# Performance work log

Hardware: AMD Instinct MI355X
Metric: run time of the kernel (lower is better)

## Reference

```python
import jax, jax.numpy as jnp
import numpy as np

D = 128
NQ = 25  # r2d2 quantized AP: 25 triangular bins over similarity range [0, 1]


def grid_sample_bilinear(img, grid):
    """F.grid_sample, mode='bilinear', padding_mode='zeros', align_corners=False.
    img: (B,C,H,W), grid: (B,Hg,Wg,2) in [-1,1] (x, y order). -> (B,C,Hg,Wg)"""
    B, C, H, W = img.shape
    gx = ((grid[..., 0] + 1.0) * W - 1.0) * 0.5  # (B,Hg,Wg) unnormalized x
    gy = ((grid[..., 1] + 1.0) * H - 1.0) * 0.5
    x0f = jnp.floor(gx)
    y0f = jnp.floor(gy)
    wx1 = gx - x0f
    wy1 = gy - y0f
    x0 = x0f.astype(jnp.int32)
    y0 = y0f.astype(jnp.int32)

    def gather(yi, xi):
        valid = ((xi >= 0) & (xi < W) & (yi >= 0) & (yi < H)).astype(img.dtype)
        xc = jnp.clip(xi, 0, W - 1)
        yc = jnp.clip(yi, 0, H - 1)
        v = jax.vmap(lambda im, y, x: im[:, y, x])(img, yc, xc)  # (B,C,Hg,Wg)
        return v * valid[:, None]

    out = (gather(y0, x0) * ((1 - wy1) * (1 - wx1))[:, None]
           + gather(y0, x0 + 1) * ((1 - wy1) * wx1)[:, None]
           + gather(y0 + 1, x0) * (wy1 * (1 - wx1))[:, None]
           + gather(y0 + 1, x0 + 1) * (wy1 * wx1)[:, None])
    return out


def quantized_ap(sim, lab):
    """r2d2 QAPLoss: soft-histogram differentiable AP.
    sim: (B,N,M) similarities, lab: (B,N,M) binary labels (float). -> (B,N) AP per query."""
    a = jnp.float32(NQ - 1)                 # slope; bin width = 1/a over gap [0,1]
    c = jnp.linspace(1.0, 0.0, NQ, dtype=sim.dtype)  # bin centers, descending score
    # triangular kernel membership: relu(1 - a*|s - c|), shape (B,N,Q,M)
    q = jnp.maximum(0.0, 1.0 - a * jnp.abs(sim[:, :, None, :] - c[None, None, :, None]))
    nbs = q.sum(-1)                          # (B,N,Q) soft count per bin
    rec = (q * lab[:, :, None, :]).sum(-1)   # (B,N,Q) soft positive count per bin
    prec = jnp.cumsum(rec, -1) / (1e-16 + jnp.cumsum(nbs, -1))
    rec = rec / rec.sum(-1, keepdims=True)
    return (prec * rec).sum(-1)              # (B,N)


def setup_inputs() -> dict:
    key = jax.random.key(0)
    k1, k2, k3, k4, k5 = jax.random.split(key, 5)
    B, H, W = 2, 32, 32
    d1 = jax.random.normal(k1, (B, D, H, W), dtype=jnp.float32)
    d2 = jax.random.normal(k2, (B, D, H, W), dtype=jnp.float32)
    # L2-normalize over channels (r2d2 descriptors are unit-norm -> sims in [-1,1])
    d1 = d1 / jnp.linalg.norm(d1, axis=1, keepdims=True)
    d2 = d2 / jnp.linalg.norm(d2, axis=1, keepdims=True)
    rel = jax.random.uniform(k3, (B, 1, H, W), dtype=jnp.float32)
    grid = jax.random.uniform(k4, (B, H, W, 2), dtype=jnp.float32) * 1.8 - 0.9  # in [-0.9,0.9]
    label = jax.random.randint(k5, (B, H, W, H, W), 0, 2, dtype=jnp.int32)
    return {"desc1": d1, "desc2": d2, "reliability": rel, "grid": grid, "label": label}


def reference(desc1, desc2, reliability, grid, label):
    B, C, H, W = desc1.shape
    d2w = grid_sample_bilinear(desc2, grid)           # warp image2 descriptors
    q = desc1.reshape(B, C, H * W).transpose(0, 2, 1)  # (B,N,C)
    db = d2w.reshape(B, C, H * W).transpose(0, 2, 1)   # (B,M,C)
    sim = jnp.einsum('bnd,bmd->bnm', q, db)            # per-sample pairwise similarity
    lab = label.reshape(B, H * W, H * W).astype(sim.dtype)
    ap = quantized_ap(sim, lab)                        # (B,N)
    return jnp.mean(ap)                                # mAP over queries and batch
```

## Files before the change

kernel.cpp:

```cpp
#include <hip/hip_runtime.h>


#define NQB 25

template<int CTRL>
__device__ __forceinline__ float dppadd(float v) {
    int s = __builtin_amdgcn_update_dpp(0, __float_as_int(v), CTRL, 0xf, 0xf, true);
    return v + __int_as_float(s);
}
__device__ __forceinline__ float red16(float v) {
    v = dppadd<0xB1>(v);
    v = dppadd<0x4E>(v);
    v = dppadd<0x141>(v);
    v = dppadd<0x140>(v);
    return v;
}

__global__ __launch_bounds__(256) void k_gs(const float* __restrict__ desc2,
                                            const float* __restrict__ grd,
                                            float* __restrict__ dbt)
{
    __shared__ float plane[1024];
    int r = blockIdx.x;
    int b = r >> 7;
    int tid = threadIdx.x;
    const float* src = desc2 + ((size_t)r << 10);
    *(float4*)&plane[tid * 4] = *(const float4*)&src[tid * 4];
    __syncthreads();
#pragma unroll
    for (int e = 0; e < 4; e++) {
        int m = tid + (e << 8);
        int pos = (b << 10) + m;
        float2 g = ((const float2*)grd)[pos];
        float fx = ((g.x + 1.f) * 32.f - 1.f) * 0.5f;
        float fy = ((g.y + 1.f) * 32.f - 1.f) * 0.5f;
        float x0f = floorf(fx), y0f = floorf(fy);
        float wx1 = fx - x0f, wy1 = fy - y0f;
        float wx0 = 1.f - wx1, wy0 = 1.f - wy1;
        int x0 = (int)x0f, y0 = (int)y0f;
        float acc = 0.f;
        if ((unsigned)y0 < 32u && (unsigned)x0 < 32u)
            acc += wy0 * wx0 * plane[(y0 << 5) + x0];
        if ((unsigned)y0 < 32u && (unsigned)(x0 + 1) < 32u)
            acc += wy0 * wx1 * plane[(y0 << 5) + x0 + 1];
        if ((unsigned)(y0 + 1) < 32u && (unsigned)x0 < 32u)
            acc += wy1 * wx0 * plane[((y0 + 1) << 5) + x0];
        if ((unsigned)(y0 + 1) < 32u && (unsigned)(x0 + 1) < 32u)
            acc += wy1 * wx1 * plane[((y0 + 1) << 5) + x0 + 1];
        dbt[((size_t)r << 10) + m] = acc;
    }
}

__global__ __launch_bounds__(512) void k_main(const float* __restrict__ desc1,
                                              const float* __restrict__ dbt,
                                              const int* __restrict__ label,
                                              float* __restrict__ appart)
{
    __shared__ float s[8][1024];
    __shared__ float CNs[8][4][NQB];
    __shared__ float CRs[8][4][NQB];
    __shared__ float apb[8];

    int tid = threadIdx.x;
    int qg0 = blockIdx.x << 3;
    int b = qg0 >> 10;
    int n0 = qg0 & 1023;

    const float* d1 = desc1 + ((size_t)b << 17) + n0;
    const float* dp = dbt + ((size_t)b << 17) + tid;

    float a0[8], a1[8];
#pragma unroll
    for (int q = 0; q < 8; q++) { a0[q] = 0.f; a1[q] = 0.f; }

#pragma unroll 2
    for (int c = 0; c < 128; c += 4) {
        float d00 = dp[(size_t)(c + 0) << 10], d01 = dp[(((size_t)(c + 0)) << 10) + 512];
        float d10 = dp[(size_t)(c + 1) << 10], d11 = dp[(((size_t)(c + 1)) << 10) + 512];
        float d20 = dp[(size_t)(c + 2) << 10], d21 = dp[(((size_t)(c + 2)) << 10) + 512];
        float d30 = dp[(size_t)(c + 3) << 10], d31 = dp[(((size_t)(c + 3)) << 10) + 512];
#pragma unroll
        for (int q = 0; q < 8; q++) {
            float qa = d1[((size_t)(c + 0) << 10) + q];
            float qb = d1[((size_t)(c + 1) << 10) + q];
            float qc = d1[((size_t)(c + 2) << 10) + q];
            float qd = d1[((size_t)(c + 3) << 10) + q];
            a0[q] = fmaf(qa, d00, fmaf(qb, d10, fmaf(qc, d20, fmaf(qd, d30, a0[q]))));
            a1[q] = fmaf(qa, d01, fmaf(qb, d11, fmaf(qc, d21, fmaf(qd, d31, a1[q]))));
        }
    }
#pragma unroll
    for (int q = 0; q < 8; q++) { s[q][tid] = a0[q]; s[q][tid + 512] = a1[q]; }
    __syncthreads();

    int q = tid >> 6, l = tid & 63;
    float CN[NQB], CR[NQB];
#pragma unroll
    for (int k = 0; k < NQB; k++) { CN[k] = 0.f; CR[k] = 0.f; }
    const int* lp = label + ((size_t)(qg0 + q) << 10) + l;
#pragma unroll
    for (int e = 0; e < 16; e++) {
        float sv = s[q][l + (e << 6)];
        float lf = (float)lp[(size_t)(e << 6)];
        float u = fmaf(-24.f, sv, 24.f);
#pragma unroll
        for (int k = 0; k < NQB; k++) {
            float t = fminf(fmaxf((float)(k + 1) - u, 0.f), 1.f);
            CN[k] += t;
            CR[k] = fmaf(lf, t, CR[k]);
        }
    }
#pragma unroll
    for (int k = 0; k < NQB; k++) { CN[k] = red16(CN[k]); CR[k] = red16(CR[k]); }
    if ((l & 15) == 0) {
        int rr = l >> 4;
#pragma unroll
        for (int k = 0; k < NQB; k++) { CNs[q][rr][k] = CN[k]; CRs[q][rr][k] = CR[k]; }
    }
    __syncthreads();

    if (tid < 8) {
        float ap = 0.f, prev = 0.f;
#pragma unroll
        for (int k = 0; k < NQB; k++) {
            float cn = CNs[tid][0][k] + CNs[tid][1][k] + CNs[tid][2][k] + CNs[tid][3][k];
            float cr = CRs[tid][0][k] + CRs[tid][1][k] + CRs[tid][2][k] + CRs[tid][3][k];
            float pr = cr / (1e-16f + cn);
            ap += pr * (cr - prev);
            prev = cr;
        }
        apb[tid] = ap / prev;
    }
    __syncthreads();
    if (tid == 0) {
        float v = 0.f;
#pragma unroll
        for (int q2 = 0; q2 < 8; q2++) v += apb[q2];
        appart[blockIdx.x] = v;
    }
}

__global__ __launch_bounds__(256) void k_final(const float* __restrict__ appart,
                                               float* __restrict__ out,
                                               int nb, float invn)
{
    int tid = threadIdx.x;
    float v = (tid < nb) ? appart[tid] : 0.f;
    for (int off = 32; off; off >>= 1) v += __shfl_xor(v, off, 64);
    __shared__ float wsum[4];
    if ((tid & 63) == 0) wsum[tid >> 6] = v;
    __syncthreads();
    if (tid == 0) out[0] = (wsum[0] + wsum[1] + wsum[2] + wsum[3]) * invn;
}

extern "C" void kernel_launch(void* const* d_in, const int* in_sizes, int n_in,
                              void* d_out, int out_size, void* d_ws, size_t ws_size,
                              hipStream_t stream)
{
    const float* desc1 = (const float*)d_in[0];
    const float* desc2 = (const float*)d_in[1];
    const float* grd   = (const float*)d_in[3];
    const int*   label = (const int*)d_in[4];

    int B = in_sizes[0] / (128 * 1024);
    int npos = B * 1024;

    float* ws = (float*)d_ws;
    float* dbt    = ws;
    float* appart = dbt + (size_t)npos * 128;
    float* out = (float*)d_out;

    k_gs<<<B * 128, 256, 0, stream>>>(desc2, grd, dbt);
    k_main<<<npos / 8, 512, 0, stream>>>(desc1, dbt, label, appart);
    k_final<<<1, 256, 0, stream>>>(appart, out, npos / 8, 1.f / (float)npos);
}
```

Measured before the change: 28.90 us.

## Use 4-query blocks with float4 db loads and early label prefetch

k_main now handles 4 queries per 256-thread block instead of 8 per 512-thread block, which doubles the grid size. Each thread computes a 4x4 register tile using a single float4 load of warped descriptors per channel. Label loads are hoisted ahead of the dot-product loop so their latency overlaps the compute. The goal is more blocks to spread across CUs and fewer load instructions, at the cost of more redundant desc1 reads per query and 16 extra registers for labels. k_final now loops over partials because their count exceeds 256.

```diff
diff --git a/kernel.cpp b/kernel.cpp
--- a/kernel.cpp
+++ b/kernel.cpp
@@ -51,75 +51,84 @@
     }
 }
 
-__global__ __launch_bounds__(512) void k_main(const float* __restrict__ desc1,
+__global__ __launch_bounds__(256) void k_main(const float* __restrict__ desc1,
                                               const float* __restrict__ dbt,
                                               const int* __restrict__ label,
                                               float* __restrict__ appart)
 {
-    __shared__ float s[8][1024];
-    __shared__ float CNs[8][4][NQB];
-    __shared__ float CRs[8][4][NQB];
-    __shared__ float apb[8];
+    __shared__ float s[4][1024];
+    __shared__ float CNs[4][4][NQB];
+    __shared__ float CRs[4][4][NQB];
+    __shared__ float apb[4];
 
     int tid = threadIdx.x;
-    int qg0 = blockIdx.x << 3;
+    int qg0 = blockIdx.x << 2;
     int b = qg0 >> 10;
     int n0 = qg0 & 1023;
 
+    int q = tid >> 6, l = tid & 63;
+    const int* lp = label + ((size_t)(qg0 + q) << 10) + l;
+    float lf[16];
+#pragma unroll
+    for (int e = 0; e < 16; e++) lf[e] = (float)lp[(size_t)(e << 6)];
+
+    const float* dp = dbt + ((size_t)b << 17) + (tid << 2);
     const float* d1 = desc1 + ((size_t)b << 17) + n0;
-    const float* dp = dbt + ((size_t)b << 17) + tid;
 
-    float a0[8], a1[8];
+    float acc[4][4];
 #pragma unroll
-    for (int q = 0; q < 8; q++) { a0[q] = 0.f; a1[q] = 0.f; }
+    for (int qq = 0; qq < 4; qq++)
+#pragma unroll
+        for (int j = 0; j < 4; j++) acc[qq][j] = 0.f;
 
-#pragma unroll 2
-    for (int c = 0; c < 128; c += 4) {
-        float d00 = dp[(size_t)(c + 0) << 10], d01 = dp[(((size_t)(c + 0)) << 10) + 512];
-        float d10 = dp[(size_t)(c + 1) << 10], d11 = dp[(((size_t)(c + 1)) << 10) + 512];
-        float d20 = dp[(size_t)(c + 2) << 10], d21 = dp[(((size_t)(c + 2)) << 10) + 512];
-        float d30 = dp[(size_t)(c + 3) << 10], d31 = dp[(((size_t)(c + 3)) << 10) + 512];
-#pragma unroll
-        for (int q = 0; q < 8; q++) {
-            float qa = d1[((size_t)(c + 0) << 10) + q];
-            float qb = d1[((size_t)(c + 1) << 10) + q];
-            float qc = d1[((size_t)(c + 2) << 10) + q];
-            float qd = d1[((size_t)(c + 3) << 10) + q];
-            a0[q] = fmaf(qa, d00, fmaf(qb, d10, fmaf(qc, d20, fmaf(qd, d30, a0[q]))));
-            a1[q] = fmaf(qa, d01, fmaf(qb, d11, fmaf(qc, d21, fmaf(qd, d31, a1[q]))));
-        }
+#pragma unroll 4
+    for (int c = 0; c < 128; c++) {
+        float4 dv = *(const float4*)&dp[(size_t)c << 10];
+        float q0 = d1[((size_t)c << 10) + 0];
+        float q1 = d1[((size_t)c << 10) + 1];
+        float q2 = d1[((size_t)c << 10) + 2];
+        float q3 = d1[((size_t)c << 10) + 3];
+        acc[0][0] = fmaf(q0, dv.x, acc[0][0]); acc[0][1] = fmaf(q0, dv.y, acc[0][1]);
+        acc[0][2] = fmaf(q0, dv.z, acc[0][2]); acc[0][3] = fmaf(q0, dv.w, acc[0][3]);
+        acc[1][0] = fmaf(q1, dv.x, acc[1][0]); acc[1][1] = fmaf(q1, dv.y, acc[1][1]);
+        acc[1][2] = fmaf(q1, dv.z, acc[1][2]); acc[1][3] = fmaf(q1, dv.w, acc[1][3]);
+        acc[2][0] = fmaf(q2, dv.x, acc[2][0]); acc[2][1] = fmaf(q2, dv.y, acc[2][1]);
+        acc[2][2] = fmaf(q2, dv.z, acc[2][2]); acc[2][3] = fmaf(q2, dv.w, acc[2][3]);
+        acc[3][0] = fmaf(q3, dv.x, acc[3][0]); acc[3][1] = fmaf(q3, dv.y, acc[3][1]);
+        acc[3][2] = fmaf(q3, dv.z, acc[3][2]); acc[3][3] = fmaf(q3, dv.w, acc[3][3]);
     }
 #pragma unroll
-    for (int q = 0; q < 8; q++) { s[q][tid] = a0[q]; s[q][tid + 512] = a1[q]; }
+    for (int qq = 0; qq < 4; qq++) {
+        float4 v; v.x = acc[qq][0]; v.y = acc[qq][1]; v.z = acc[qq][2]; v.w = acc[qq][3];
+        *(float4*)&s[qq][tid << 2] = v;
+    }
     __syncthreads();
 
-    int q = tid >> 6, l = tid & 63;
     float CN[NQB], CR[NQB];
 #pragma unroll
     for (int k = 0; k < NQB; k++) { CN[k] = 0.f; CR[k] = 0.f; }
-    const int* lp = label + ((size_t)(qg0 + q) << 10) + l;
 #pragma unroll
     for (int e = 0; e < 16; e++) {
         float sv = s[q][l + (e << 6)];
-        float lf = (float)lp[(size_t)(e << 6)];
         float u = fmaf(-24.f, sv, 24.f);
+        float lfv = lf[e];
 #pragma unroll
         for (int k = 0; k < NQB; k++) {
             float t = fminf(fmaxf((float)(k + 1) - u, 0.f), 1.f);
             CN[k] += t;
-            CR[k] = fmaf(lf, t, CR[k]);
+            CR[k] = fmaf(lfv, t, CR[k]);
         }
     }
 #pragma unroll
     for (int k = 0; k < NQB; k++) { CN[k] = red16(CN[k]); CR[k] = red16(CR[k]); }
     if ((l & 15) == 0) {
-        int rr = l >> 4;
+        int rec = l >> 4;
 #pragma unroll
-        for (int k = 0; k < NQB; k++) { CNs[q][rr][k] = CN[k]; CRs[q][rr][k] = CR[k]; }
+        for (int k = 0; k < NQB; k++) { CNs[q][rec][k] = CN[k]; CRs[q][rec][k] = CR[k]; }
     }
     __syncthreads();
 
-    if (tid < 8) {
+    if (tid < 4) {
         float ap = 0.f, prev = 0.f;
 #pragma unroll
         for (int k = 0; k < NQB; k++) {
@@ -132,12 +141,7 @@
         apb[tid] = ap / prev;
     }
     __syncthreads();
-    if (tid == 0) {
-        float v = 0.f;
-#pragma unroll
-        for (int q2 = 0; q2 < 8; q2++) v += apb[q2];
-        appart[blockIdx.x] = v;
-    }
+    if (tid == 0) appart[blockIdx.x] = apb[0] + apb[1] + apb[2] + apb[3];
 }
 
 __global__ __launch_bounds__(256) void k_final(const float* __restrict__ appart,
@@ -145,7 +149,8 @@
                                                int nb, float invn)
 {
     int tid = threadIdx.x;
-    float v = (tid < nb) ? appart[tid] : 0.f;
+    float v = 0.f;
+    for (int i = tid; i < nb; i += 256) v += appart[i];
     for (int off = 32; off; off >>= 1) v += __shfl_xor(v, off, 64);
     __shared__ float wsum[4];
     if ((tid & 63) == 0) wsum[tid >> 6] = v;
@@ -171,6 +176,6 @@
     float* out = (float*)d_out;
 
     k_gs<<<B * 128, 256, 0, stream>>>(desc2, grd, dbt);
-    k_main<<<npos / 8, 512, 0, stream>>>(desc1, dbt, label, appart);
-    k_final<<<1, 256, 0, stream>>>(appart, out, npos / 8, 1.f / (float)npos);
+    k_main<<<npos / 4, 256, 0, stream>>>(desc1, dbt, label, appart);
+    k_final<<<1, 256, 0, stream>>>(appart, out, npos / 4, 1.f / (float)npos);
 }
```

Result: slower. 33.77 us (+16.9%).
